# Kernel optimization log

Measured on AMD Instinct MI355X. Metric: run time of the kernel, lower is better.

Reference implementation:

```python
import jax, jax.numpy as jnp
import numpy as np

VOCAB = 100000
EMB = 128
B = 16384
W_POS = 10
K_NEG = 64


def setup_inputs() -> dict:
    key = jax.random.key(0)
    k1, k2, k3, k4, k5 = jax.random.split(key, 5)
    return {
        "input": jax.random.randint(k1, (B,), 0, VOCAB),
        "pos_labels": jax.random.randint(k2, (B, W_POS), 0, VOCAB),
        "neg_labels": jax.random.randint(k3, (B, K_NEG), 0, VOCAB),
        # nn.Embedding weights init'd uniform(-1, 1) (padding row overwritten too)
        "input_emb": jax.random.uniform(k4, (VOCAB, EMB), jnp.float32, -1.0, 1.0),
        "output_emb": jax.random.uniform(k5, (VOCAB, EMB), jnp.float32, -1.0, 1.0),
    }


def reference(input, pos_labels, neg_labels, input_emb, output_emb):
    # Embedding gathers
    center = input_emb[input]            # [B, D]
    pos = output_emb[pos_labels]         # [B, W, D]
    neg = output_emb[neg_labels]         # [B, K, D]
    # Batched dot products: bmm(pos, center.unsqueeze(2)).squeeze(2)
    pos_dot = jnp.einsum("bwd,bd->bw", pos, center)
    neg_dot = jnp.einsum("bkd,bd->bk", neg, center)
    # NOTE: original code applies logsigmoid to neg_dot directly (no negation),
    # faithfully reproduced here.
    log_pos = jax.nn.log_sigmoid(pos_dot).sum(axis=1)  # [B]
    log_neg = jax.nn.log_sigmoid(neg_dot).sum(axis=1)  # [B]
    loss = -(log_pos + log_neg)
    return loss.sum(axis=0)
```

## Files before the change

### kernel.cpp

```cpp
#include <hip/hip_runtime.h>


#define VOCAB  100000
#define EMB    128
#define B_TOT  16384
#define W_POS  10
#define K_NEG  64
#define N_LAB  (W_POS + K_NEG)
#define NCHUNK 19
#define DEPTH  8

__device__ __forceinline__ float logsig(float x) {
    const float e = __expf(-fabsf(x));
    return fminf(x, 0.0f) - 0.69314718056f * __log2f(1.0f + e);
}

__global__ __launch_bounds__(256, 4) void skipgram_kernel(
    const int*   __restrict__ input,
    const int*   __restrict__ pos_labels,
    const int*   __restrict__ neg_labels,
    const float* __restrict__ input_emb,
    const float* __restrict__ output_emb,
    float*       __restrict__ out)
{
    const int lane = threadIdx.x & 63;
    const int gl   = lane & 15;
    const int grp  = lane >> 4;
    const int wave = (int)((blockIdx.x * blockDim.x + threadIdx.x) >> 6);
    const int b    = wave;

    const int* pl = pos_labels + b * W_POS;
    const int* nl = neg_labels + b * K_NEG;

    int idx[NCHUNK];
    #pragma unroll
    for (int t = 0; t < NCHUNK; ++t) {
        const int j = 4 * t + grp;
        idx[t] = (j < W_POS) ? pl[j] : ((j < N_LAB) ? nl[j - W_POS] : 0);
    }

    const int c = input[b];
    const float4* crow = (const float4*)(input_emb + (size_t)c * EMB);
    const float4 c0 = crow[gl * 2], c1 = crow[gl * 2 + 1];

    float4 A[DEPTH][2];
    #pragma unroll
    for (int t = 0; t < DEPTH; ++t) {
        const float4* rp = (const float4*)(output_emb + (size_t)idx[t] * EMB);
        A[t][0] = rp[gl * 2];
        A[t][1] = rp[gl * 2 + 1];
    }

    float acc = 0.0f;

    #pragma unroll
    for (int t = 0; t < NCHUNK; ++t) {
        const float4 a0 = A[t % DEPTH][0];
        const float4 a1 = A[t % DEPTH][1];

        if (t + DEPTH < NCHUNK) {
            const float4* rp =
                (const float4*)(output_emb + (size_t)idx[t + DEPTH] * EMB);
            A[t % DEPTH][0] = rp[gl * 2];
            A[t % DEPTH][1] = rp[gl * 2 + 1];
        }

        float p = a0.x * c0.x + a0.y * c0.y + a0.z * c0.z + a0.w * c0.w
                + a1.x * c1.x + a1.y * c1.y + a1.z * c1.z + a1.w * c1.w;

        p += __shfl_xor(p, 1);
        p += __shfl_xor(p, 2);
        p += __shfl_xor(p, 4);
        p += __shfl_xor(p, 8);

        const int j = 4 * t + grp;
        if (gl == 0 && j < N_LAB) acc += logsig(p);
    }

    acc += __shfl_xor(acc, 16);
    acc += __shfl_xor(acc, 32);

    __shared__ float part[4];
    if (lane == 0) part[threadIdx.x >> 6] = acc;
    __syncthreads();
    if (threadIdx.x == 0) {
        const float s = part[0] + part[1] + part[2] + part[3];
        atomicAdd(out, -s);
    }
}

extern "C" void kernel_launch(void* const* d_in, const int* in_sizes, int n_in,
                              void* d_out, int out_size, void* d_ws, size_t ws_size,
                              hipStream_t stream) {
    const int*   input      = (const int*)  d_in[0];
    const int*   pos_labels = (const int*)  d_in[1];
    const int*   neg_labels = (const int*)  d_in[2];
    const float* input_emb  = (const float*)d_in[3];
    const float* output_emb = (const float*)d_in[4];
    float*       out        = (float*)      d_out;

    hipMemsetAsync(out, 0, sizeof(float), stream);

    dim3 grid(4096), block(256);
    hipLaunchKernelGGL(skipgram_kernel, grid, block, 0, stream,
                       input, pos_labels, neg_labels, input_emb, output_emb, out);
}
```

Baseline: 91.97 us.

## Stream gathered embedding rows into an LDS ring via async global-to-LDS loads

Replaces the register-held prefetch of output-embedding rows with `global_load_lds` transfers into a per-wave 7-slot LDS ring buffer. Loads are issued 6 chunks ahead and gated by explicit `vmcnt` waits and scheduling barriers. The aim is to free vector registers and keep more loads in flight without register pressure. In exchange it uses about 57KB of LDS per block and drops the occupancy hint, which can cut resident blocks per CU and reduce overall memory-level parallelism.

```diff
diff --git a/kernel.cpp b/kernel.cpp
--- a/kernel.cpp
+++ b/kernel.cpp
@@ -8,14 +8,22 @@
 #define K_NEG  64
 #define N_LAB  (W_POS + K_NEG)
 #define NCHUNK 19
-#define DEPTH  8
+#define DEPTH  6
+#define NBUF   7
 
 __device__ __forceinline__ float logsig(float x) {
     const float e = __expf(-fabsf(x));
     return fminf(x, 0.0f) - 0.69314718056f * __log2f(1.0f + e);
 }
 
-__global__ __launch_bounds__(256, 4) void skipgram_kernel(
+__device__ __forceinline__ void gload_lds16(const float* g, float* l) {
+    __builtin_amdgcn_global_load_lds(
+        (const __attribute__((address_space(1))) unsigned int*)g,
+        (__attribute__((address_space(3))) unsigned int*)l,
+        16, 0, 0);
+}
+
+__global__ __launch_bounds__(256) void skipgram_kernel(
     const int*   __restrict__ input,
     const int*   __restrict__ pos_labels,
     const int*   __restrict__ neg_labels,
@@ -23,9 +31,12 @@
     const float* __restrict__ output_emb,
     float*       __restrict__ out)
 {
+    __shared__ __align__(16) float buf[4][NBUF][2][256];
+
     const int lane = threadIdx.x & 63;
     const int gl   = lane & 15;
     const int grp  = lane >> 4;
+    const int w    = threadIdx.x >> 6;
     const int wave = (int)((blockIdx.x * blockDim.x + threadIdx.x) >> 6);
     const int b    = wave;
 
@@ -43,45 +54,51 @@
     const float4* crow = (const float4*)(input_emb + (size_t)c * EMB);
     const float4 c0 = crow[gl * 2], c1 = crow[gl * 2 + 1];
 
-    float4 A[DEPTH][2];
-    #pragma unroll
-    for (int t = 0; t < DEPTH; ++t) {
-        const float4* rp = (const float4*)(output_emb + (size_t)idx[t] * EMB);
-        A[t][0] = rp[gl * 2];
-        A[t][1] = rp[gl * 2 + 1];
-    }
-
     float acc = 0.0f;
 
-    #pragma unroll
-    for (int t = 0; t < NCHUNK; ++t) {
-        const float4 a0 = A[t % DEPTH][0];
-        const float4 a1 = A[t % DEPTH][1];
+#define ISSUE(t) do {                                                        \
+        if ((t) < NCHUNK) {                                                  \
+            const float* g0 = output_emb + (size_t)idx[(t)] * EMB + gl * 8;  \
+            gload_lds16(g0,     &buf[w][(t) % NBUF][0][0]);                  \
+            gload_lds16(g0 + 4, &buf[w][(t) % NBUF][1][0]);                  \
+        }                                                                    \
+    } while (0)
 
-        if (t + DEPTH < NCHUNK) {
-            const float4* rp =
-                (const float4*)(output_emb + (size_t)idx[t + DEPTH] * EMB);
-            A[t % DEPTH][0] = rp[gl * 2];
-            A[t % DEPTH][1] = rp[gl * 2 + 1];
-        }
+#define STEP(t, vm) do {                                                     \
+        asm volatile("s_waitcnt vmcnt(" #vm ")" ::: "memory");               \
+        __builtin_amdgcn_sched_barrier(0);                                   \
+        const float4 a0 = *(const float4*)&buf[w][(t) % NBUF][0][lane * 4];  \
+        const float4 a1 = *(const float4*)&buf[w][(t) % NBUF][1][lane * 4];  \
+        asm volatile("s_waitcnt lgkmcnt(0)" ::: "memory");                   \
+        __builtin_amdgcn_sched_barrier(0);                                   \
+        ISSUE((t) + DEPTH);                                                  \
+        float p = a0.x * c0.x + a0.y * c0.y + a0.z * c0.z + a0.w * c0.w      \
+                + a1.x * c1.x + a1.y * c1.y + a1.z * c1.z + a1.w * c1.w;     \
+        p += __shfl_xor(p, 1);                                               \
+        p += __shfl_xor(p, 2);                                               \
+        p += __shfl_xor(p, 4);                                               \
+        p += __shfl_xor(p, 8);                                               \
+        const int j = 4 * (t) + grp;                                         \
+        if (gl == 0 && j < N_LAB) acc += logsig(p);                          \
+    } while (0)
 
-        float p = a0.x * c0.x + a0.y * c0.y + a0.z * c0.z + a0.w * c0.w
-                + a1.x * c1.x + a1.y * c1.y + a1.z * c1.z + a1.w * c1.w;
+    ISSUE(0); ISSUE(1); ISSUE(2); ISSUE(3); ISSUE(4); ISSUE(5);
 
-        p += __shfl_xor(p, 1);
-        p += __shfl_xor(p, 2);
-        p += __shfl_xor(p, 4);
-        p += __shfl_xor(p, 8);
+    STEP(0, 12);  STEP(1, 12);  STEP(2, 12);  STEP(3, 12);
+    STEP(4, 12);  STEP(5, 12);  STEP(6, 12);  STEP(7, 12);
+    STEP(8, 12);  STEP(9, 12);  STEP(10, 12); STEP(11, 12);
+    STEP(12, 12);
+    STEP(13, 10); STEP(14, 8);  STEP(15, 6);  STEP(16, 4);
+    STEP(17, 2);  STEP(18, 0);
 
-        const int j = 4 * t + grp;
-        if (gl == 0 && j < N_LAB) acc += logsig(p);
-    }
+#undef STEP
+#undef ISSUE
 
     acc += __shfl_xor(acc, 16);
     acc += __shfl_xor(acc, 32);
 
     __shared__ float part[4];
-    if (lane == 0) part[threadIdx.x >> 6] = acc;
+    if (lane == 0) part[w] = acc;
     __syncthreads();
     if (threadIdx.x == 0) {
         const float s = part[0] + part[1] + part[2] + part[3];
```

Result: slower. 98.89 us (+7.5%).
